# Kernel optimization log

Measured on AMD Instinct MI355X. Metric: run time of the kernel, lower is better.

## Reference

```python
import jax, jax.numpy as jnp
import numpy as np

TAU = 0.05       # sinkhorn temperature (functools.partial in GCN_Net)
SK_ITERS = 20    # sinkhorn max_iter


def _mlp(x, w1, b1, w2, b2):
    # nn.Sequential(Linear, ReLU, Linear)
    return jnp.maximum(x @ w1 + b1, 0.0) @ w2 + b2


def _cosine(f1, f2, eps=1e-8):
    # torch CosineSimilarity over broadcast (E1,1,D) x (1,E2,D), computed as a GEMM
    n1 = jnp.maximum(jnp.linalg.norm(f1, axis=-1), eps)
    n2 = jnp.maximum(jnp.linalg.norm(f2, axis=-1), eps)
    return (f1 @ f2.T) / (n1[:, None] * n2[None, :])


def _sinkhorn(s):
    # log-domain sinkhorn, alternating row/col normalization (pygmtools-style)
    log_s = s / TAU
    for i in range(SK_ITERS):
        log_s = log_s - jax.nn.logsumexp(log_s, axis=(1 if i % 2 == 0 else 0), keepdims=True)
    return jnp.exp(log_s)


def _build_conn_edges(preds):
    # fully-connected off-diagonal graph; edge feats [dx, dy, dist, cls_src, cls_dst]
    n = preds.shape[0]
    pos = preds[:, 1:3]
    cls = preds[:, 6]
    idx = np.arange(n)
    r, c = np.meshgrid(idx, idx, indexing='ij')
    m = r != c
    conn = np.stack([r[m], c[m]], axis=1)  # (E,2), static under jit
    src, dst = conn[:, 0], conn[:, 1]
    d = pos[dst] - pos[src]                             # (E,2)
    dist = jnp.linalg.norm(d, axis=-1, keepdims=True)   # (E,1)
    edges = jnp.concatenate([d, dist, cls[src][:, None], cls[dst][:, None]], axis=-1)  # (E,5)
    return jnp.asarray(conn), edges


def _forward(ego_preds, cav_preds, node_w1, node_b1, node_w2, node_b2,
             edge_w1, edge_b1, edge_w2, edge_b2,
             l0_self_w, l0_self_b, l0_conv_w, l0_conv_b, l0_cls_w, l0_cls_b,
             l1_self_w, l1_self_b, l1_conv_w, l1_conv_b, l1_cls_w, l1_cls_b,
             fc_w, fc_b):
    ego = ego_preds[0]
    cav = cav_preds[0]
    n1, n2 = ego.shape[0], cav.shape[0]
    conn1, e1 = _build_conn_edges(ego)
    conn2, e2 = _build_conn_edges(cav)
    # --- NodeMLP affinity ---
    f1 = _mlp(ego[:, 1:6], node_w1, node_b1, node_w2, node_b2)
    f2 = _mlp(cav[:, 1:6], node_w1, node_b1, node_w2, node_b2)
    cls_eq = (ego[:, 6][:, None] == cav[:, 6][None, :]).astype(ego.dtype)
    conf = jnp.sum(jnp.sqrt(ego[:, 7:][:, None, :] * cav[:, 7:][None, :, :]), axis=-1)
    node_aff = cls_eq * conf * _cosine(f1, f2)                         # (n1,n2)
    # --- EdgeMLP affinity ---
    g1 = _mlp(e1[:, :3], edge_w1, edge_b1, edge_w2, edge_b2)
    g2 = _mlp(e2[:, :3], edge_w1, edge_b1, edge_w2, edge_b2)
    ecls = jnp.all(e1[:, 3:].astype(jnp.int32)[:, None, :] == e2[:, 3:].astype(jnp.int32)[None, :, :],
                   axis=-1).astype(ego.dtype)
    edge_aff = ecls * _cosine(g1, g2)                                  # (E1,E2)
    # --- Lawler affinity matrix K over association graph: node (i,a) -> i*n2+a ---
    N = n1 * n2
    rows = (conn1[:, 0][:, None] * n2 + conn2[:, 0][None, :]).ravel()
    cols = (conn1[:, 1][:, None] * n2 + conn2[:, 1][None, :]).ravel()
    K = jnp.zeros((N, N), ego.dtype).at[rows, cols].set(edge_aff.ravel())
    d_idx = jnp.arange(N)
    K = K.at[d_idx, d_idx].set(node_aff.ravel())
    # --- GCN adjacency = nonzero pattern of K, with added self-loops + sym norm ---
    A = (K != 0).astype(ego.dtype) + jnp.eye(N, dtype=ego.dtype)
    dinv = jax.lax.rsqrt(A.sum(axis=1))
    normA = dinv[:, None] * A * dinv[None, :]
    x = jnp.diag(K)[:, None]                                           # (N,1)
    # --- NGMConvLayers: self-loop Linear + GCNConv + sinkhorn channel ---
    for sw, sb, cw, cb, kw, kb in (
            (l0_self_w, l0_self_b, l0_conv_w, l0_conv_b, l0_cls_w, l0_cls_b),
            (l1_self_w, l1_self_b, l1_conv_w, l1_conv_b, l1_cls_w, l1_cls_b)):
        x = (x @ sw + sb) + (normA @ (x @ cw) + cb)
        sk = _sinkhorn((x @ kw + kb).reshape(n1, n2))
        x = x + sk.reshape(-1, 1)
    scores = x @ fc_w + fc_b                                           # (N,1)
    s = scores.reshape(n2, n1).T                                       # view(n2,-1).t()
    return _sinkhorn(s)


def setup_inputs() -> dict:
    key = jax.random.key(0)
    ks = jax.random.split(key, 16)

    def lin(k, fi, fo):
        kw, kb = jax.random.split(k)
        s = (2.0 / (fi + fo)) ** 0.5
        return (jax.random.normal(kw, (fi, fo), jnp.float32) * s,
                jax.random.normal(kb, (fo,), jnp.float32) * 0.01)

    def make_preds(k, n):
        k1, k2 = jax.random.split(k)
        p = jax.random.uniform(k1, (1, n, 8), jnp.float32)
        cls = jnp.floor(jax.random.uniform(k2, (1, n)) * 3.0)  # 3 discrete classes
        p = p.at[:, :, 6].set(cls)
        p = p.at[:, :, 7].set(0.1 + 0.9 * p[:, :, 7])          # positive confidences
        return p

    inp = {'ego_preds': make_preds(ks[0], 64), 'cav_preds': make_preds(ks[1], 64)}
    inp['node_w1'], inp['node_b1'] = lin(ks[2], 5, 64)
    inp['node_w2'], inp['node_b2'] = lin(ks[3], 64, 32)
    inp['edge_w1'], inp['edge_b1'] = lin(ks[4], 3, 64)
    inp['edge_w2'], inp['edge_b2'] = lin(ks[5], 64, 32)
    inp['l0_self_w'], inp['l0_self_b'] = lin(ks[6], 1, 16)
    inp['l0_conv_w'], inp['l0_conv_b'] = lin(ks[7], 1, 16)
    inp['l0_cls_w'], inp['l0_cls_b'] = lin(ks[8], 16, 1)
    inp['l1_self_w'], inp['l1_self_b'] = lin(ks[9], 16, 16)
    inp['l1_conv_w'], inp['l1_conv_b'] = lin(ks[10], 16, 16)
    inp['l1_cls_w'], inp['l1_cls_b'] = lin(ks[11], 16, 1)
    inp['fc_w'], inp['fc_b'] = lin(ks[12], 16, 1)
    return inp


def reference(ego_preds, cav_preds, node_w1, node_b1, node_w2, node_b2,
              edge_w1, edge_b1, edge_w2, edge_b2,
              l0_self_w, l0_self_b, l0_conv_w, l0_conv_b, l0_cls_w, l0_cls_b,
              l1_self_w, l1_self_b, l1_conv_w, l1_conv_b, l1_cls_w, l1_cls_b,
              fc_w, fc_b):
    return _forward(ego_preds, cav_preds, node_w1, node_b1, node_w2, node_b2,
                    edge_w1, edge_b1, edge_w2, edge_b2,
                    l0_self_w, l0_self_b, l0_conv_w, l0_conv_b, l0_cls_w, l0_cls_b,
                    l1_self_w, l1_self_b, l1_conv_w, l1_conv_b, l1_cls_w, l1_cls_b,
                    fc_w, fc_b)
```

## Files before the change

kernel.cpp:

```cpp
#include <hip/hip_runtime.h>
#include <math.h>


#define SK_SCALE 28.853900817779268f

template<int CTRL>
__device__ __forceinline__ float dppf(float x) {
    int xi = __float_as_int(x);
    int rr = __builtin_amdgcn_update_dpp(xi, xi, CTRL, 0xF, 0xF, false);
    return __int_as_float(rr);
}
__device__ __forceinline__ float quad_sum(float v) {
    v += dppf<0xB1>(v); v += dppf<0x4E>(v); return v;
}
__device__ __forceinline__ float quad_max(float v) {
    v = fmaxf(v, dppf<0xB1>(v)); v = fmaxf(v, dppf<0x4E>(v)); return v;
}
__device__ __forceinline__ float e2f(float x) { return __builtin_amdgcn_exp2f(x); }
__device__ __forceinline__ float rcpf(float x) { return __builtin_amdgcn_rcpf(x); }
__device__ __forceinline__ float dot4(const float4 a, const float4 b) {
    return a.x*b.x + a.y*b.y + a.z*b.z + a.w*b.w;
}
__device__ __forceinline__ void fma4(float4& a, float b, const float4 c) {
    a.x += b*c.x; a.y += b*c.y; a.z += b*c.z; a.w += b*c.w;
}
__device__ __forceinline__ void add4(float4& a, const float4 c) {
    a.x += c.x; a.y += c.y; a.z += c.z; a.w += c.w;
}
__device__ __forceinline__ void ld16(const float* p, float* o) {
    #pragma unroll
    for (int t = 0; t < 4; ++t) {
        float4 v = *(const float4*)(p + 4*t);
        o[4*t+0]=v.x; o[4*t+1]=v.y; o[4*t+2]=v.z; o[4*t+3]=v.w;
    }
}
__device__ __forceinline__ float dotsum16(const float* a, const float* b) {
    float s0=0,s1=0,s2=0,s3=0;
    #pragma unroll
    for (int t = 0; t < 4; ++t) {
        s0 += a[4*t+0]*b[4*t+0]; s1 += a[4*t+1]*b[4*t+1];
        s2 += a[4*t+2]*b[4*t+2]; s3 += a[4*t+3]*b[4*t+3];
    }
    return (s0+s1)+(s2+s3);
}
__device__ __forceinline__ float sum16(const float* a) {
    float s0=0,s1=0,s2=0,s3=0;
    #pragma unroll
    for (int t = 0; t < 4; ++t) {
        s0 += a[4*t+0]; s1 += a[4*t+1]; s2 += a[4*t+2]; s3 += a[4*t+3];
    }
    return (s0+s1)+(s2+s3);
}
__device__ __forceinline__ void stage16(float* dst, const float* v, float sc) {
    #pragma unroll
    for (int t = 0; t < 4; ++t)
        *(float4*)(dst + 4*t) = make_float4(v[4*t+0]*sc, v[4*t+1]*sc,
                                            v[4*t+2]*sc, v[4*t+3]*sc);
}
__device__ __forceinline__ float sel4(const float* v, int q) {
    float w = v[0];
    w = (q == 1) ? v[1] : w;
    w = (q == 2) ? v[2] : w;
    w = (q == 3) ? v[3] : w;
    return w;
}

__device__ __forceinline__ void sk_pre(const float* tq, const float* tt, int r, int q,
                                       float* AN, float* AT, float* up, float* rmp) {
    float m0 = tq[0];
    #pragma unroll
    for (int j = 1; j < 16; ++j) m0 = fmaxf(m0, tq[j]);
    float rm = quad_max(m0);
    float a[16];
    #pragma unroll
    for (int j = 0; j < 16; ++j) a[j] = e2f(tq[j] - rm);
    stage16(AN + r*68 + 16*q, a, 1.0f);
    float u = rcpf(quad_sum(sum16(a)));
    if (q == 0) { rmp[r] = rm; up[r] = u; }
    __syncthreads();
    float rmq[16]; ld16(rmp + 16*q, rmq);
    float at[16];
    #pragma unroll
    for (int j = 0; j < 16; ++j) at[j] = e2f(tt[j] - rmq[j]);
    stage16(AT + r*68 + 16*q, at, 1.0f);
    __syncthreads();
}

__device__ __forceinline__ void sk_iter_wave0(const float* AN, const float* AT,
                                              float* up, float* vp, int lane,
                                              float* outp) {
    const int rr = lane >> 2, q = lane & 3;
    float us[4], vs[4];
    #pragma unroll 1
    for (int p = 0; p < 9; ++p) {
        float uq[16]; ld16(up + 16*q, uq);
        #pragma unroll
        for (int s = 0; s < 4; ++s) {
            float a[16]; ld16(AT + (16*s + rr)*68 + 16*q, a);
            vs[s] = quad_sum(dotsum16(a, uq));
        }
        vp[16*q + rr] = rcpf(sel4(vs, q));
        float vq[16]; ld16(vp + 16*q, vq);
        #pragma unroll
        for (int s = 0; s < 4; ++s) {
            float a[16]; ld16(AN + (16*s + rr)*68 + 16*q, a);
            us[s] = quad_sum(dotsum16(a, vq));
        }
        up[16*q + rr] = rcpf(sel4(us, q));
    }
    {
        float uq[16]; ld16(up + 16*q, uq);
        #pragma unroll
        for (int s = 0; s < 4; ++s) {
            float a[16]; ld16(AT + (16*s + rr)*68 + 16*q, a);
            vs[s] = quad_sum(dotsum16(a, uq));
        }
        vp[16*q + rr] = rcpf(sel4(vs, q));
    }
    if (outp) {
        float vq[16]; ld16(vp + 16*q, vq);
        #pragma unroll
        for (int s = 0; s < 4; ++s) {
            float uR = rcpf(us[s]);
            float a[16]; ld16(AN + (16*s + rr)*68 + 16*q, a);
            #pragma unroll
            for (int t = 0; t < 4; ++t) {
                float4 o4;
                o4.x = a[4*t+0] * uR * vq[4*t+0];
                o4.y = a[4*t+1] * uR * vq[4*t+1];
                o4.z = a[4*t+2] * uR * vq[4*t+2];
                o4.w = a[4*t+3] * uR * vq[4*t+3];
                *(float4*)(outp + (16*s + rr)*64 + 16*q + 4*t) = o4;
            }
        }
    }
}

__device__ __forceinline__ void sk_recon(const float* AN, const float* AT, int r, int q,
                                         const float* up, const float* vp,
                                         float* sv, float* st) {
    float ur = up[r], vr = vp[r];
    float uq[16], vq[16], an[16], at[16];
    ld16(up + 16*q, uq); ld16(vp + 16*q, vq);
    ld16(AN + r*68 + 16*q, an); ld16(AT + r*68 + 16*q, at);
    #pragma unroll
    for (int m = 0; m < 16; ++m) {
        sv[m] = an[m] * ur * vq[m];
        st[m] = at[m] * uq[m] * vr;
    }
}

__device__ __forceinline__ void matvec_dual(const float* u1, const float* u1t,
                                            const float* u2, const float* u2t,
                                            const float* mmq, const float* dqv,
                                            const float* mmt, const float* dqt,
                                            float* o1, float* o1t, float* o2, float* o2t,
                                            int q, int r,
                                            float* WR1, float* WC1, float* WR2, float* WC2) {
    float rs1=0, rs2=0, cs1=0, cs2=0;
    #pragma unroll
    for (int m = 0; m < 16; ++m) {
        float md = mmq[m]*dqv[m], mdt = mmt[m]*dqt[m];
        rs1 += md * u1[m];               cs1 += mdt * u1t[m];
        rs2 += md * (u2 ? u2[m] : 1.0f); cs2 += mdt * (u2t ? u2t[m] : 1.0f);
    }
    rs1 = quad_sum(rs1); rs2 = quad_sum(rs2);
    cs1 = quad_sum(cs1); cs2 = quad_sum(cs2);
    if (q == 0) { WR1[r]=rs1; WR2[r]=rs2; WC1[r]=cs1; WC2[r]=cs2; }
    __syncthreads();
    float wr1[16], wc1[16], wr2[16], wc2[16];
    ld16(WR1 + 16*q, wr1); ld16(WC1 + 16*q, wc1);
    ld16(WR2 + 16*q, wr2); ld16(WC2 + 16*q, wc2);
    float W1 = quad_sum(sum16(wc1));
    float W2 = quad_sum(sum16(wc2));
    #pragma unroll
    for (int m = 0; m < 16; ++m) {
        float d = dqv[m], mm = mmq[m];
        float u1m = u1[m], u2m = u2 ? u2[m] : 1.0f;
        float z1 = mm*d*u1m, z2 = mm*d*u2m;
        o1[m] = d*((1.0f+mm)*d*u1m + mm*(W1 - rs1 - wc1[m] + z1));
        o2[m] = d*((1.0f+mm)*d*u2m + mm*(W2 - rs2 - wc2[m] + z2));
        float dt = dqt[m], mt = mmt[m];
        float u1tm = u1t[m], u2tm = u2t ? u2t[m] : 1.0f;
        float z1t = mt*dt*u1tm, z2t = mt*dt*u2tm;
        o1t[m] = dt*((1.0f+mt)*dt*u1tm + mt*(W1 - wr1[m] - cs1 + z1t));
        o2t[m] = dt*((1.0f+mt)*dt*u2tm + mt*(W2 - wr2[m] - cs2 + z2t));
    }
}

extern "C" __global__ __launch_bounds__(256, 1)
void gcn_match_kernel(const float* ego, const float* cav,
                      const float* nw1, const float* nb1, const float* nw2, const float* nb2,
                      const float* sw0, const float* sb0, const float* cw0, const float* cb0,
                      const float* kw0, const float* kb0,
                      const float* sw1, const float* sb1, const float* cw1, const float* cb1,
                      const float* kw1, const float* kb1,
                      const float* fcw, const float* fcb,
                      float* out) {
    __shared__ __align__(16) float sh_hT1[64 * 68];
    __shared__ __align__(16) float sh_hT2[64 * 68];
    __shared__ __align__(16) float sh_w2[2048];
    __shared__ __align__(16) float sh_f1[64 * 36];
    __shared__ __align__(16) float sh_f2[64 * 36];
    __shared__ __align__(16) float sh_nw1[320];
    __shared__ __align__(16) float sh_nb1[64], sh_nb2[32];
    __shared__ __align__(16) float sh_cls1[64], sh_cf1[64], sh_cls2[64], sh_cf2[64];
    __shared__ __align__(16) float sh_n1[64], sh_n2[64], sh_Dr[64], sh_Dc[64];
    __shared__ __align__(16) float sh_up[64], sh_vp[64], sh_rmp[64];
    __shared__ __align__(16) float sh_WR1[64], sh_WC1[64], sh_WR2[64], sh_WC2[64];
    __shared__ __align__(16) float sh_sw0[16], sh_sb0[16], sh_cw0[16], sh_cb0[16];
    __shared__ __align__(16) float sh_sb1[16], sh_cb1[16];
    __shared__ __align__(16) float sh_sw1[256], sh_cw1[256];
    __shared__ __align__(16) float sh_kw0[16], sh_kw1[16], sh_fcw[16];
    __shared__ float sh_kb[4];
    __shared__ float sh_avec[7 * 16];
    __shared__ float sh_coef[18];

    const int tid = threadIdx.x;
    const int wv = tid >> 6, lane = tid & 63;
    const int r = tid >> 2, q = tid & 3;

    ((float4*)sh_w2)[tid]       = ((const float4*)nw2)[tid];
    ((float4*)sh_w2)[tid + 256] = ((const float4*)nw2)[tid + 256];
    if (tid < 80)       ((float4*)sh_nw1)[tid]      = ((const float4*)nw1)[tid];
    else if (tid < 96)  ((float4*)sh_nb1)[tid-80]   = ((const float4*)nb1)[tid-80];
    else if (tid < 104) ((float4*)sh_nb2)[tid-96]   = ((const float4*)nb2)[tid-96];
    else if (tid < 108) ((float4*)sh_sw0)[tid-104]  = ((const float4*)sw0)[tid-104];
    else if (tid < 112) ((float4*)sh_sb0)[tid-108]  = ((const float4*)sb0)[tid-108];
    else if (tid < 116) ((float4*)sh_cw0)[tid-112]  = ((const float4*)cw0)[tid-112];
    else if (tid < 120) ((float4*)sh_cb0)[tid-116]  = ((const float4*)cb0)[tid-116];
    else if (tid < 124) ((float4*)sh_sb1)[tid-120]  = ((const float4*)sb1)[tid-120];
    else if (tid < 128) ((float4*)sh_cb1)[tid-124]  = ((const float4*)cb1)[tid-124];
    else if (tid < 192) ((float4*)sh_sw1)[tid-128]  = ((const float4*)sw1)[tid-128];
    else                ((float4*)sh_cw1)[tid-192]  = ((const float4*)cw1)[tid-192];
    if (tid < 4)        ((float4*)sh_kw0)[tid]      = ((const float4*)kw0)[tid];
    else if (tid < 8)   ((float4*)sh_kw1)[tid-4]    = ((const float4*)kw1)[tid-4];
    else if (tid < 12)  ((float4*)sh_fcw)[tid-8]    = ((const float4*)fcw)[tid-8];
    else if (tid == 12) sh_kb[0] = kb0[0];
    else if (tid == 13) sh_kb[1] = kb1[0];
    else if (tid == 14) sh_kb[2] = fcb[0];
    if (tid < 64) { sh_cls1[tid] = ego[tid*8+6]; sh_cf1[tid] = ego[tid*8+7]; }
    else if (tid < 128) { int j = tid-64; sh_cls2[j] = cav[j*8+6]; sh_cf2[j] = cav[j*8+7]; }
    __syncthreads();

    {
        float4 ea = ((const float4*)ego)[lane*2], eb = ((const float4*)ego)[lane*2+1];
        float4 ca = ((const float4*)cav)[lane*2], cb = ((const float4*)cav)[lane*2+1];
        #pragma unroll
        for (int kk = 0; kk < 16; ++kk) {
            int k = 16*wv + kk;
            float b1 = sh_nb1[k];
            float w0 = sh_nw1[k],       w1 = sh_nw1[64+k],  w2_ = sh_nw1[128+k];
            float w3 = sh_nw1[192+k],   w4 = sh_nw1[256+k];
            sh_hT1[k*68 + lane] = fmaxf(b1 + ea.y*w0 + ea.z*w1 + ea.w*w2_ + eb.x*w3 + eb.y*w4, 0.0f);
            sh_hT2[k*68 + lane] = fmaxf(b1 + ca.y*w0 + ca.z*w1 + ca.w*w2_ + cb.x*w3 + cb.y*w4, 0.0f);
        }
    }
    __syncthreads();

    if (wv < 2) {
        const float* HT = (wv == 0) ? sh_hT1 : sh_hT2;
        float* F  = (wv == 0) ? sh_f1 : sh_f2;
        float* NN = (wv == 0) ? sh_n1 : sh_n2;
        const int rr = lane >> 2, oq = lane & 3;
        float4 accA[4], accB[4];
        #pragma unroll
        for (int m = 0; m < 4; ++m) { accA[m] = make_float4(0,0,0,0); accB[m] = accA[m]; }
        #pragma unroll 4
        for (int k = 0; k < 64; ++k) {
            float4 hq = *(const float4*)(HT + k*68 + 4*rr);
            float4 wA = *(const float4*)(sh_w2 + k*32 + 4*oq);
            float4 wB = *(const float4*)(sh_w2 + k*32 + 16 + 4*oq);
            fma4(accA[0], hq.x, wA); fma4(accB[0], hq.x, wB);
            fma4(accA[1], hq.y, wA); fma4(accB[1], hq.y, wB);
            fma4(accA[2], hq.z, wA); fma4(accB[2], hq.z, wB);
            fma4(accA[3], hq.w, wA); fma4(accB[3], hq.w, wB);
        }
        float4 b2a = *(const float4*)(sh_nb2 + 4*oq);
        float4 b2b = *(const float4*)(sh_nb2 + 16 + 4*oq);
        float sq[4];
        #pragma unroll
        for (int m = 0; m < 4; ++m) {
            add4(accA[m], b2a); add4(accB[m], b2b);
            int row = 4*rr + m;
            *(float4*)(F + row*36 + 4*oq)      = accA[m];
            *(float4*)(F + row*36 + 16 + 4*oq) = accB[m];
            float q2 = dot4(accA[m], accA[m]) + dot4(accB[m], accB[m]);
            q2 += dppf<0xB1>(q2); q2 += dppf<0x4E>(q2);
            sq[m] = q2;
        }
        if (oq == 0) {
            #pragma unroll
            for (int m = 0; m < 4; ++m)
                NN[4*rr + m] = fmaxf(sqrtf(sq[m]), 1e-8f);
        }
    } else if (wv == 2) {
        if (lane < 16) {
            int o = lane;
            float ax=0, av=0, as_=0, aw=0, au=0, ae=0, a1=0;
            #pragma unroll
            for (int k = 0; k < 16; ++k) {
                float s0k = sh_sw0[k], c0k = sh_cw0[k], b0k = sh_sb0[k] + sh_cb0[k];
                float s1ko = sh_sw1[k*16+o], c1ko = sh_cw1[k*16+o];
                ax += s0k*s1ko;  av += c0k*s1ko + s0k*c1ko;  as_ += s1ko;
                aw += c0k*c1ko;  au += c1ko;  ae += b0k*c1ko;  a1 += b0k*s1ko;
            }
            a1 += sh_sb1[o] + sh_cb1[o];
            sh_avec[0*16+o]=ax; sh_avec[1*16+o]=av; sh_avec[2*16+o]=as_;
            sh_avec[3*16+o]=aw; sh_avec[4*16+o]=au; sh_avec[5*16+o]=ae;
            sh_avec[6*16+o]=a1;
        }
        if (lane < 18) {
            int t = lane; float c = 0.0f;
            if (t == 0)      { for (int k = 0; k < 16; ++k) c += sh_sw0[k]*sh_kw0[k]; }
            else if (t == 1) { for (int k = 0; k < 16; ++k) c += sh_cw0[k]*sh_kw0[k]; }
            else if (t == 2) { for (int k = 0; k < 16; ++k) c += (sh_sb0[k]+sh_cb0[k])*sh_kw0[k]; c += sh_kb[0]; }
            else if (t < 10) { int v = t-3;
                for (int o = 0; o < 16; ++o) c += sh_avec[v*16+o]*sh_kw1[o];
                if (v == 6) c += sh_kb[1];
            } else if (t < 17) { int v = t-10;
                for (int o = 0; o < 16; ++o) c += sh_avec[v*16+o]*sh_fcw[o];
                if (v == 6) c += sh_kb[2];
            } else { for (int o = 0; o < 16; ++o) c += sh_fcw[o]; }
            sh_coef[t] = c;
        }
    }
    __syncthreads();

    {
        const int sc = lane & 15, rc = lane >> 4;
        float dt[4][4];
        #pragma unroll
        for (int m = 0; m < 4; ++m)
            #pragma unroll
            for (int k = 0; k < 4; ++k) dt[m][k] = 0.0f;
        for (int kq = 0; kq < 8; ++kq) {
            float4 f2q[4];
            #pragma unroll
            for (int k = 0; k < 4; ++k)
                f2q[k] = *(const float4*)(sh_f2 + (sc + 16*k)*36 + 4*kq);
            #pragma unroll
            for (int m = 0; m < 4; ++m) {
                int rrow = 16*m + 4*wv + rc;
                float4 f1q = *(const float4*)(sh_f1 + rrow*36 + 4*kq);
                #pragma unroll
                for (int k = 0; k < 4; ++k) dt[m][k] += dot4(f1q, f2q[k]);
            }
        }
        #pragma unroll
        for (int m = 0; m < 4; ++m) {
            int rrow = 16*m + 4*wv + rc;
            #pragma unroll
            for (int k = 0; k < 4; ++k) {
                sh_hT1[rrow*68 + sc + 16*k] = dt[m][k];
                sh_hT2[(sc + 16*k)*68 + rrow] = dt[m][k];
            }
        }
    }
    float mmq[16], mmt[16], cfq[16], cft[16];
    float Drr, Dcr;
    {
        float c2q[16], c1q[16], f2v[16], f1v[16];
        ld16(sh_cls2 + 16*q, c2q); ld16(sh_cls1 + 16*q, c1q);
        ld16(sh_cf2 + 16*q, f2v);  ld16(sh_cf1 + 16*q, f1v);
        const float cls1r = sh_cls1[r], cls2r = sh_cls2[r];
        const float cf1r = sh_cf1[r],  cf2r  = sh_cf2[r];
        float dr = 0, dc = 0;
        #pragma unroll
        for (int m = 0; m < 16; ++m) {
            mmq[m] = (cls1r == c2q[m]) ? 1.0f : 0.0f;
            mmt[m] = (c1q[m] == cls2r) ? 1.0f : 0.0f;
            dr += mmq[m]; dc += mmt[m];
            cfq[m] = sqrtf(cf1r * f2v[m]);
            cft[m] = sqrtf(f1v[m] * cf2r);
        }
        Drr = quad_sum(dr);
        Dcr = quad_sum(dc);
        if (q == 0) { sh_Dr[r] = Drr; sh_Dc[r] = Dcr; }
    }
    __syncthreads();

    float dqv[16], dqt[16], x0[16], x0t[16];
    {
        float dcq[16], drq[16], n2q[16], n1q[16], dotq[16], dotTq[16];
        ld16(sh_Dc + 16*q, dcq); ld16(sh_Dr + 16*q, drq);
        ld16(sh_n2 + 16*q, n2q); ld16(sh_n1 + 16*q, n1q);
        ld16(sh_hT1 + r*68 + 16*q, dotq);
        ld16(sh_hT2 + r*68 + 16*q, dotTq);
        float Tdeg = quad_sum(sum16(dcq));
        const float n1r = sh_n1[r], n2r = sh_n2[r];
        #pragma unroll
        for (int m = 0; m < 16; ++m) {
            dqv[m] = (mmq[m] != 0.0f) ? (1.0f / sqrtf(Tdeg - Drr - dcq[m] + 3.0f)) : 1.0f;
            dqt[m] = (mmt[m] != 0.0f) ? (1.0f / sqrtf(Tdeg - drq[m] - Dcr + 3.0f)) : 1.0f;
            x0[m]  = mmq[m] * cfq[m] * (dotq[m]  / (n1r * n2q[m]));
            x0t[m] = mmt[m] * cft[m] * (dotTq[m] / (n1q[m] * n2r));
        }
    }

    float v0[16], v0t[16], oe[16], oet[16];
    matvec_dual(x0, x0t, nullptr, nullptr, mmq, dqv, mmt, dqt,
                v0, v0t, oe, oet, q, r, sh_WR1, sh_WC1, sh_WR2, sh_WC2);

    float t0q[16], t0t[16], t1b[16], t1bt[16], sbse[16], sbst[16];
    {
        float c0 = sh_coef[0], c1 = sh_coef[1], c2 = sh_coef[2];
        float ctx = sh_coef[3], ctv = sh_coef[4];
        float ce_ = sh_coef[8], ct1 = sh_coef[9];
        float csx = sh_coef[10], csv = sh_coef[11];
        float ce2 = sh_coef[15], cs1 = sh_coef[16];
        #pragma unroll
        for (int m = 0; m < 16; ++m) {
            t0q[m] = (c0*x0[m]  + c1*v0[m]  + c2) * SK_SCALE;
            t0t[m] = (c0*x0t[m] + c1*v0t[m] + c2) * SK_SCALE;
            t1b[m]  = ctx*x0[m]  + ctv*v0[m]  + ct1 + ce_*oe[m];
            t1bt[m] = ctx*x0t[m] + ctv*v0t[m] + ct1 + ce_*oet[m];
            sbse[m] = csx*x0[m]  + csv*v0[m]  + cs1 + ce2*oe[m];
            sbst[m] = csx*x0t[m] + csv*v0t[m] + cs1 + ce2*oet[m];
        }
    }

    sk_pre(t0q, t0t, r, q, sh_hT1, sh_hT2, sh_up, sh_rmp);
    if (wv == 0) sk_iter_wave0(sh_hT1, sh_hT2, sh_up, sh_vp, lane, nullptr);
    __syncthreads();
    float s0v[16], s0t[16];
    sk_recon(sh_hT1, sh_hT2, r, q, sh_up, sh_vp, s0v, s0t);

    float ov[16], ovt[16], os[16], ost[16];
    matvec_dual(v0, v0t, s0v, s0t, mmq, dqv, mmt, dqt,
                ov, ovt, os, ost, q, r, sh_WR1, sh_WC1, sh_WR2, sh_WC2);
    float t1q[16], t1t[16], sacc[16], sacct[16];
    {
        float cts = sh_coef[5], cw_ = sh_coef[6], cu_ = sh_coef[7];
        float css = sh_coef[12], cw2 = sh_coef[13], cu2 = sh_coef[14];
        #pragma unroll
        for (int m = 0; m < 16; ++m) {
            t1q[m] = (t1b[m]  + cts*s0v[m] + cw_*ov[m]  + cu_*os[m])  * SK_SCALE;
            t1t[m] = (t1bt[m] + cts*s0t[m] + cw_*ovt[m] + cu_*ost[m]) * SK_SCALE;
            sacc[m]  = sbse[m] + css*s0v[m] + cw2*ov[m]  + cu2*os[m];
            sacct[m] = sbst[m] + css*s0t[m] + cw2*ovt[m] + cu2*ost[m];
        }
    }

    sk_pre(t1q, t1t, r, q, sh_hT1, sh_hT2, sh_up, sh_rmp);
    if (wv == 0) sk_iter_wave0(sh_hT1, sh_hT2, sh_up, sh_vp, lane, nullptr);
    __syncthreads();
    {
        float c17 = sh_coef[17];
        float s1v[16], s1t[16];
        sk_recon(sh_hT1, sh_hT2, r, q, sh_up, sh_vp, s1v, s1t);
        #pragma unroll
        for (int m = 0; m < 16; ++m) {
            sacc[m]  += c17 * s1v[m];
            sacct[m] += c17 * s1t[m];
        }
    }
    __syncthreads();

    {
        float t2q[16], t2t[16];
        #pragma unroll
        for (int m = 0; m < 16; ++m) {
            t2q[m] = sacct[m] * SK_SCALE;
            t2t[m] = sacc[m] * SK_SCALE;
        }
        sk_pre(t2q, t2t, r, q, sh_hT1, sh_hT2, sh_up, sh_rmp);
        if (wv == 0) sk_iter_wave0(sh_hT1, sh_hT2, sh_up, sh_vp, lane, out);
    }
}

extern "C" void kernel_launch(void* const* d_in, const int* in_sizes, int n_in,
                              void* d_out, int out_size, void* d_ws, size_t ws_size,
                              hipStream_t stream) {
    const float* ego = (const float*)d_in[0];
    const float* cav = (const float*)d_in[1];
    const float* nw1 = (const float*)d_in[2];
    const float* nb1 = (const float*)d_in[3];
    const float* nw2 = (const float*)d_in[4];
    const float* nb2 = (const float*)d_in[5];
    const float* sw0 = (const float*)d_in[10];
    const float* sb0 = (const float*)d_in[11];
    const float* cw0 = (const float*)d_in[12];
    const float* cb0 = (const float*)d_in[13];
    const float* kw0 = (const float*)d_in[14];
    const float* kb0 = (const float*)d_in[15];
    const float* sw1 = (const float*)d_in[16];
    const float* sb1 = (const float*)d_in[17];
    const float* cw1 = (const float*)d_in[18];
    const float* cb1 = (const float*)d_in[19];
    const float* kw1 = (const float*)d_in[20];
    const float* kb1 = (const float*)d_in[21];
    const float* fcw = (const float*)d_in[22];
    const float* fcb = (const float*)d_in[23];

    gcn_match_kernel<<<dim3(1), dim3(256), 0, stream>>>(
        ego, cav, nw1, nb1, nw2, nb2,
        sw0, sb0, cw0, cb0, kw0, kb0,
        sw1, sb1, cw1, cb1, kw1, kb1,
        fcw, fcb, (float*)d_out);
}
```

Baseline: 134.1 us.

## Keep Sinkhorn matrices in registers and spill intermediates to shared memory

The Sinkhorn iteration loop now loads the normalized and transposed affinity tiles into registers once, instead of re-reading them from shared memory on every iteration. To make room for those registers, long-lived per-thread arrays (t1b, sbse, v0, sacc and their transposes) are staged into a reused shared scratch buffer. Transposed copies are re-read via strided loads rather than computed in parallel. The mask and degree arrays are recomputed after the first Sinkhorn pass instead of being kept live. This trades extra shared-memory traffic and recomputation for lower register pressure and fewer LDS reads in the serial single-wave Sinkhorn loop.

```diff
diff --git a/kernel.cpp b/kernel.cpp
--- a/kernel.cpp
+++ b/kernel.cpp
@@ -33,6 +33,10 @@
         float4 v = *(const float4*)(p + 4*t);
         o[4*t+0]=v.x; o[4*t+1]=v.y; o[4*t+2]=v.z; o[4*t+3]=v.w;
     }
+}
+__device__ __forceinline__ void ldT(const float* X, int r, int q, float* o) {
+    #pragma unroll
+    for (int m = 0; m < 16; ++m) o[m] = X[(16*q + m)*64 + r];
 }
 __device__ __forceinline__ float dotsum16(const float* a, const float* b) {
     float s0=0,s1=0,s2=0,s3=0;
@@ -86,35 +90,32 @@
     __syncthreads();
 }
 
-__device__ __forceinline__ void sk_iter_wave0(const float* AN, const float* AT,
-                                              float* up, float* vp, int lane,
-                                              float* outp) {
+__device__ __forceinline__ void sk_iter_reg(const float* AN, const float* AT,
+                                            float* up, float* vp, int lane,
+                                            float* outp) {
     const int rr = lane >> 2, q = lane & 3;
+    float aq[4][16], att[4][16];
+    #pragma unroll
+    for (int s = 0; s < 4; ++s) {
+        ld16(AN + (16*s + rr)*68 + 16*q, aq[s]);
+        ld16(AT + (16*s + rr)*68 + 16*q, att[s]);
+    }
     float us[4], vs[4];
     #pragma unroll 1
     for (int p = 0; p < 9; ++p) {
         float uq[16]; ld16(up + 16*q, uq);
         #pragma unroll
-        for (int s = 0; s < 4; ++s) {
-            float a[16]; ld16(AT + (16*s + rr)*68 + 16*q, a);
-            vs[s] = quad_sum(dotsum16(a, uq));
-        }
+        for (int s = 0; s < 4; ++s) vs[s] = quad_sum(dotsum16(att[s], uq));
         vp[16*q + rr] = rcpf(sel4(vs, q));
         float vq[16]; ld16(vp + 16*q, vq);
         #pragma unroll
-        for (int s = 0; s < 4; ++s) {
-            float a[16]; ld16(AN + (16*s + rr)*68 + 16*q, a);
-            us[s] = quad_sum(dotsum16(a, vq));
-        }
+        for (int s = 0; s < 4; ++s) us[s] = quad_sum(dotsum16(aq[s], vq));
         up[16*q + rr] = rcpf(sel4(us, q));
     }
     {
         float uq[16]; ld16(up + 16*q, uq);
         #pragma unroll
-        for (int s = 0; s < 4; ++s) {
-            float a[16]; ld16(AT + (16*s + rr)*68 + 16*q, a);
-            vs[s] = quad_sum(dotsum16(a, uq));
-        }
+        for (int s = 0; s < 4; ++s) vs[s] = quad_sum(dotsum16(att[s], uq));
         vp[16*q + rr] = rcpf(sel4(vs, q));
     }
     if (outp) {
@@ -122,14 +123,13 @@
         #pragma unroll
         for (int s = 0; s < 4; ++s) {
             float uR = rcpf(us[s]);
-            float a[16]; ld16(AN + (16*s + rr)*68 + 16*q, a);
             #pragma unroll
             for (int t = 0; t < 4; ++t) {
                 float4 o4;
-                o4.x = a[4*t+0] * uR * vq[4*t+0];
-                o4.y = a[4*t+1] * uR * vq[4*t+1];
-                o4.z = a[4*t+2] * uR * vq[4*t+2];
-                o4.w = a[4*t+3] * uR * vq[4*t+3];
+                o4.x = aq[s][4*t+0] * uR * vq[4*t+0];
+                o4.y = aq[s][4*t+1] * uR * vq[4*t+1];
+                o4.z = aq[s][4*t+2] * uR * vq[4*t+2];
+                o4.w = aq[s][4*t+3] * uR * vq[4*t+3];
                 *(float4*)(outp + (16*s + rr)*64 + 16*q + 4*t) = o4;
             }
         }
@@ -199,9 +199,13 @@
                       float* out) {
     __shared__ __align__(16) float sh_hT1[64 * 68];
     __shared__ __align__(16) float sh_hT2[64 * 68];
-    __shared__ __align__(16) float sh_w2[2048];
-    __shared__ __align__(16) float sh_f1[64 * 36];
-    __shared__ __align__(16) float sh_f2[64 * 36];
+    __shared__ __align__(16) float sh_scr[12288];
+    float* const SH_W2  = sh_scr;
+    float* const SH_F1  = sh_scr + 2048;
+    float* const SH_F2  = sh_scr + 4352;
+    float* const SH_T1B = sh_scr;
+    float* const SH_SB  = sh_scr + 4096;
+    float* const SH_V0  = sh_scr + 8192;
     __shared__ __align__(16) float sh_nw1[320];
     __shared__ __align__(16) float sh_nb1[64], sh_nb2[32];
     __shared__ __align__(16) float sh_cls1[64], sh_cf1[64], sh_cls2[64], sh_cf2[64];
@@ -220,8 +224,8 @@
     const int wv = tid >> 6, lane = tid & 63;
     const int r = tid >> 2, q = tid & 3;
 
-    ((float4*)sh_w2)[tid]       = ((const float4*)nw2)[tid];
-    ((float4*)sh_w2)[tid + 256] = ((const float4*)nw2)[tid + 256];
+    ((float4*)SH_W2)[tid]       = ((const float4*)nw2)[tid];
+    ((float4*)SH_W2)[tid + 256] = ((const float4*)nw2)[tid + 256];
     if (tid < 80)       ((float4*)sh_nw1)[tid]      = ((const float4*)nw1)[tid];
     else if (tid < 96)  ((float4*)sh_nb1)[tid-80]   = ((const float4*)nb1)[tid-80];
     else if (tid < 104) ((float4*)sh_nb2)[tid-96]   = ((const float4*)nb2)[tid-96];
@@ -260,7 +264,7 @@
 
     if (wv < 2) {
         const float* HT = (wv == 0) ? sh_hT1 : sh_hT2;
-        float* F  = (wv == 0) ? sh_f1 : sh_f2;
+        float* F  = (wv == 0) ? SH_F1 : SH_F2;
         float* NN = (wv == 0) ? sh_n1 : sh_n2;
         const int rr = lane >> 2, oq = lane & 3;
         float4 accA[4], accB[4];
@@ -269,8 +273,8 @@
         #pragma unroll 4
         for (int k = 0; k < 64; ++k) {
             float4 hq = *(const float4*)(HT + k*68 + 4*rr);
-            float4 wA = *(const float4*)(sh_w2 + k*32 + 4*oq);
-            float4 wB = *(const float4*)(sh_w2 + k*32 + 16 + 4*oq);
+            float4 wA = *(const float4*)(SH_W2 + k*32 + 4*oq);
+            float4 wB = *(const float4*)(SH_W2 + k*32 + 16 + 4*oq);
             fma4(accA[0], hq.x, wA); fma4(accB[0], hq.x, wB);
             fma4(accA[1], hq.y, wA); fma4(accB[1], hq.y, wB);
             fma4(accA[2], hq.z, wA); fma4(accB[2], hq.z, wB);
@@ -338,11 +342,11 @@
             float4 f2q[4];
             #pragma unroll
             for (int k = 0; k < 4; ++k)
-                f2q[k] = *(const float4*)(sh_f2 + (sc + 16*k)*36 + 4*kq);
+                f2q[k] = *(const float4*)(SH_F2 + (sc + 16*k)*36 + 4*kq);
             #pragma unroll
             for (int m = 0; m < 4; ++m) {
                 int rrow = 16*m + 4*wv + rc;
-                float4 f1q = *(const float4*)(sh_f1 + rrow*36 + 4*kq);
+                float4 f1q = *(const float4*)(SH_F1 + rrow*36 + 4*kq);
                 #pragma unroll
                 for (int k = 0; k < 4; ++k) dt[m][k] += dot4(f1q, f2q[k]);
             }
@@ -402,71 +406,100 @@
     matvec_dual(x0, x0t, nullptr, nullptr, mmq, dqv, mmt, dqt,
                 v0, v0t, oe, oet, q, r, sh_WR1, sh_WC1, sh_WR2, sh_WC2);
 
-    float t0q[16], t0t[16], t1b[16], t1bt[16], sbse[16], sbst[16];
+    float t0q[16], t0t[16];
     {
         float c0 = sh_coef[0], c1 = sh_coef[1], c2 = sh_coef[2];
         float ctx = sh_coef[3], ctv = sh_coef[4];
         float ce_ = sh_coef[8], ct1 = sh_coef[9];
         float csx = sh_coef[10], csv = sh_coef[11];
         float ce2 = sh_coef[15], cs1 = sh_coef[16];
+        float t1b[16], sbse[16];
         #pragma unroll
         for (int m = 0; m < 16; ++m) {
             t0q[m] = (c0*x0[m]  + c1*v0[m]  + c2) * SK_SCALE;
             t0t[m] = (c0*x0t[m] + c1*v0t[m] + c2) * SK_SCALE;
             t1b[m]  = ctx*x0[m]  + ctv*v0[m]  + ct1 + ce_*oe[m];
-            t1bt[m] = ctx*x0t[m] + ctv*v0t[m] + ct1 + ce_*oet[m];
             sbse[m] = csx*x0[m]  + csv*v0[m]  + cs1 + ce2*oe[m];
-            sbst[m] = csx*x0t[m] + csv*v0t[m] + cs1 + ce2*oet[m];
-        }
+        }
+        stage16(SH_T1B + r*64 + 16*q, t1b, 1.0f);
+        stage16(SH_SB  + r*64 + 16*q, sbse, 1.0f);
+        stage16(SH_V0  + r*64 + 16*q, v0, 1.0f);
     }
 
     sk_pre(t0q, t0t, r, q, sh_hT1, sh_hT2, sh_up, sh_rmp);
-    if (wv == 0) sk_iter_wave0(sh_hT1, sh_hT2, sh_up, sh_vp, lane, nullptr);
+    if (wv == 0) sk_iter_reg(sh_hT1, sh_hT2, sh_up, sh_vp, lane, nullptr);
     __syncthreads();
     float s0v[16], s0t[16];
     sk_recon(sh_hT1, sh_hT2, r, q, sh_up, sh_vp, s0v, s0t);
+
+    {
+        float c2q[16], c1q[16];
+        ld16(sh_cls2 + 16*q, c2q); ld16(sh_cls1 + 16*q, c1q);
+        const float cls1r = sh_cls1[r], cls2r = sh_cls2[r];
+        #pragma unroll
+        for (int m = 0; m < 16; ++m) {
+            mmq[m] = (cls1r == c2q[m]) ? 1.0f : 0.0f;
+            mmt[m] = (c1q[m] == cls2r) ? 1.0f : 0.0f;
+        }
+        float dcq[16], drq[16];
+        ld16(sh_Dc + 16*q, dcq); ld16(sh_Dr + 16*q, drq);
+        float Tdeg = quad_sum(sum16(dcq));
+        const float Dr2 = sh_Dr[r], Dc2 = sh_Dc[r];
+        #pragma unroll
+        for (int m = 0; m < 16; ++m) {
+            dqv[m] = (mmq[m] != 0.0f) ? (1.0f / sqrtf(Tdeg - Dr2 - dcq[m] + 3.0f)) : 1.0f;
+            dqt[m] = (mmt[m] != 0.0f) ? (1.0f / sqrtf(Tdeg - drq[m] - Dc2 + 3.0f)) : 1.0f;
+        }
+    }
+    {
+        float v0n[16], v0tn[16];
+        ld16(SH_V0 + r*64 + 16*q, v0n);
+        ldT(SH_V0, r, q, v0tn);
+        #pragma unroll
+        for (int m = 0; m < 16; ++m) { v0[m] = v0n[m]; v0t[m] = v0tn[m]; }
+    }
 
     float ov[16], ovt[16], os[16], ost[16];
     matvec_dual(v0, v0t, s0v, s0t, mmq, dqv, mmt, dqt,
                 ov, ovt, os, ost, q, r, sh_WR1, sh_WC1, sh_WR2, sh_WC2);
-    float t1q[16], t1t[16], sacc[16], sacct[16];
+    float t1q[16], t1t[16];
     {
         float cts = sh_coef[5], cw_ = sh_coef[6], cu_ = sh_coef[7];
         float css = sh_coef[12], cw2 = sh_coef[13], cu2 = sh_coef[14];
-        #pragma unroll
-        for (int m = 0; m < 16; ++m) {
-            t1q[m] = (t1b[m]  + cts*s0v[m] + cw_*ov[m]  + cu_*os[m])  * SK_SCALE;
-            t1t[m] = (t1bt[m] + cts*s0t[m] + cw_*ovt[m] + cu_*ost[m]) * SK_SCALE;
-            sacc[m]  = sbse[m] + css*s0v[m] + cw2*ov[m]  + cu2*os[m];
-            sacct[m] = sbst[m] + css*s0t[m] + cw2*ovt[m] + cu2*ost[m];
-        }
+        float t1b_[16], t1bt_[16], sbse_[16], sacc[16];
+        ld16(SH_T1B + r*64 + 16*q, t1b_);
+        ldT(SH_T1B, r, q, t1bt_);
+        ld16(SH_SB + r*64 + 16*q, sbse_);
+        #pragma unroll
+        for (int m = 0; m < 16; ++m) {
+            t1q[m] = (t1b_[m]  + cts*s0v[m] + cw_*ov[m]  + cu_*os[m])  * SK_SCALE;
+            t1t[m] = (t1bt_[m] + cts*s0t[m] + cw_*ovt[m] + cu_*ost[m]) * SK_SCALE;
+            sacc[m] = sbse_[m] + css*s0v[m] + cw2*ov[m]  + cu2*os[m];
+        }
+        stage16(SH_V0 + r*64 + 16*q, sacc, 1.0f);
     }
 
     sk_pre(t1q, t1t, r, q, sh_hT1, sh_hT2, sh_up, sh_rmp);
-    if (wv == 0) sk_iter_wave0(sh_hT1, sh_hT2, sh_up, sh_vp, lane, nullptr);
-    __syncthreads();
+    if (wv == 0) sk_iter_reg(sh_hT1, sh_hT2, sh_up, sh_vp, lane, nullptr);
+    __syncthreads();
+    float t2q[16], t2t[16];
     {
         float c17 = sh_coef[17];
         float s1v[16], s1t[16];
         sk_recon(sh_hT1, sh_hT2, r, q, sh_up, sh_vp, s1v, s1t);
-        #pragma unroll
-        for (int m = 0; m < 16; ++m) {
-            sacc[m]  += c17 * s1v[m];
-            sacct[m] += c17 * s1t[m];
-        }
-    }
-    __syncthreads();
-
-    {
-        float t2q[16], t2t[16];
-        #pragma unroll
-        for (int m = 0; m < 16; ++m) {
-            t2q[m] = sacct[m] * SK_SCALE;
-            t2t[m] = sacc[m] * SK_SCALE;
-        }
-        sk_pre(t2q, t2t, r, q, sh_hT1, sh_hT2, sh_up, sh_rmp);
-        if (wv == 0) sk_iter_wave0(sh_hT1, sh_hT2, sh_up, sh_vp, lane, out);
-    }
+        float saccN[16], saccT[16];
+        ld16(SH_V0 + r*64 + 16*q, saccN);
+        ldT(SH_V0, r, q, saccT);
+        #pragma unroll
+        for (int m = 0; m < 16; ++m) {
+            t2q[m] = (saccT[m] + c17 * s1t[m]) * SK_SCALE;
+            t2t[m] = (saccN[m] + c17 * s1v[m]) * SK_SCALE;
+        }
+    }
+    __syncthreads();
+
+    sk_pre(t2q, t2t, r, q, sh_hT1, sh_hT2, sh_up, sh_rmp);
+    if (wv == 0) sk_iter_reg(sh_hT1, sh_hT2, sh_up, sh_vp, lane, out);
 }
 
 extern "C" void kernel_launch(void* const* d_in, const int* in_sizes, int n_in,
```

New measurement: 136.1 us. Within noise of the previous version (+1.5%).
